# Kernel optimization log

Measured on AMD Instinct MI355X. Metric: run time of the kernel, lower is better.

The kernel has to match this reference:

```python
import jax, jax.numpy as jnp
import numpy as np

N0, N1, N2 = 360448, 22528, 2048
E0, E1 = 337920, 20480
D = 256


def setup_inputs() -> dict:
    key = jax.random.key(0)
    ks = jax.random.split(key, 12)
    s = 1.0 / np.sqrt(D)
    return {
        "x": jax.random.normal(ks[0], (N0, D), dtype=jnp.float32),
        "src0": jax.random.randint(ks[1], (E0,), 0, N0, dtype=jnp.int32),
        "dst0": jax.random.randint(ks[2], (E0,), 0, N1, dtype=jnp.int32),
        "src1": jax.random.randint(ks[3], (E1,), 0, N1, dtype=jnp.int32),
        "dst1": jax.random.randint(ks[4], (E1,), 0, N2, dtype=jnp.int32),
        "Wl0": jax.random.normal(ks[5], (D, D), dtype=jnp.float32) * s,
        "bl0": jnp.zeros((D,), dtype=jnp.float32),
        "Wr0": jax.random.normal(ks[6], (D, D), dtype=jnp.float32) * s,
        "Wl1": jax.random.normal(ks[7], (D, D), dtype=jnp.float32) * s,
        "bl1": jnp.zeros((D,), dtype=jnp.float32),
        "Wr1": jax.random.normal(ks[8], (D, D), dtype=jnp.float32) * s,
    }


def _sage_conv(x_src, x_tgt, src, dst, n_tgt, Wl, bl, Wr):
    # mean aggregation of source neighbor features per target node
    summed = jax.ops.segment_sum(x_src[src], dst, num_segments=n_tgt)
    cnt = jax.ops.segment_sum(jnp.ones((src.shape[0],), x_src.dtype), dst,
                              num_segments=n_tgt)
    agg = summed / jnp.maximum(cnt, 1.0)[:, None]
    # PyG SAGEConv: lin_l(agg) + lin_r(x_target); lin_r has no bias
    return agg @ Wl.T + bl + x_tgt @ Wr.T


def reference(x, src0, dst0, src1, dst1, Wl0, bl0, Wr0, Wl1, bl1, Wr1):
    # layer 0: [N0, D] -> [N1, D]
    h = _sage_conv(x, x[:N1], src0, dst0, N1, Wl0, bl0, Wr0)
    h = jax.nn.relu(h)  # dropout is identity in eval mode
    # layer 1: [N1, D] -> [N2, D]
    out = _sage_conv(h, h[:N2], src1, dst1, N2, Wl1, bl1, Wr1)
    return out
```

## Files before the change

### kernel.cpp

```cpp
#include <hip/hip_runtime.h>
#include <hip/hip_bf16.h>

#define N1C 22528
#define N2C 2048

typedef __attribute__((ext_vector_type(8))) short bf16x8;
typedef __attribute__((ext_vector_type(4))) float f32x4;

__device__ __forceinline__ short f2bf(float f) {
    union { float f; unsigned u; } x; x.f = f;
    unsigned r = x.u + 0x7fff + ((x.u >> 16) & 1);
    return (short)(r >> 16);
}
__device__ __forceinline__ float bf2f(unsigned short u) {
    union { unsigned u; float f; } x; x.u = ((unsigned)u) << 16;
    return x.f;
}

__global__ void prep_kernel(const float* __restrict__ Wl0, const float* __restrict__ Wr0,
                            const float* __restrict__ Wl1, const float* __restrict__ Wr1,
                            short* __restrict__ Wcat0, short* __restrict__ Wcat1,
                            int* __restrict__ hist0, int* __restrict__ hist1) {
    const int stride = gridDim.x * blockDim.x;
    const int tid0 = blockIdx.x * blockDim.x + threadIdx.x;
    for (int i = tid0; i < 2 * 256 * 512; i += stride) {
        int layer = i >> 17;
        int r = i & ((1 << 17) - 1);
        int j = r >> 9, k = r & 511;
        const float* Wl = layer ? Wl1 : Wl0;
        const float* Wr = layer ? Wr1 : Wr0;
        float v = (k < 256) ? Wl[j * 256 + k] : Wr[j * 256 + (k - 256)];
        (layer ? Wcat1 : Wcat0)[r] = f2bf(v);
    }
    for (int i = tid0; i < N1C + N2C; i += stride) {
        if (i < N1C) hist0[i] = 0; else hist1[i - N1C] = 0;
    }
}

__global__ void hist_both_kernel(const int* __restrict__ dst0, int E0,
                                 const int* __restrict__ dst1, int E1,
                                 int* __restrict__ hist0, int* __restrict__ hist1) {
    const int stride = gridDim.x * blockDim.x;
    for (int i = blockIdx.x * blockDim.x + threadIdx.x; i < E0 + E1; i += stride) {
        if (i < E0) atomicAdd(&hist0[dst0[i]], 1);
        else        atomicAdd(&hist1[dst1[i - E0]], 1);
    }
}

__global__ __launch_bounds__(1024)
void scan_both_kernel(const int* __restrict__ hist0, int* __restrict__ rowptr0,
                      int* __restrict__ cursor0,
                      const int* __restrict__ hist1, int* __restrict__ rowptr1,
                      int* __restrict__ cursor1) {
    __shared__ int sums[1024];
    const int N = (blockIdx.x == 0) ? N1C : N2C;
    const int* hist   = (blockIdx.x == 0) ? hist0 : hist1;
    int* rowptr       = (blockIdx.x == 0) ? rowptr0 : rowptr1;
    int* cursor       = (blockIdx.x == 0) ? cursor0 : cursor1;
    const int tid = threadIdx.x;
    const int per = (N + 1023) >> 10;
    const int start = tid * per;
    const int end = min(start + per, N);
    int s = 0;
    for (int i = start; i < end; ++i) s += hist[i];
    sums[tid] = s;
    __syncthreads();
    for (int d = 1; d < 1024; d <<= 1) {
        int t = (tid >= d) ? sums[tid - d] : 0;
        __syncthreads();
        sums[tid] += t;
        __syncthreads();
    }
    int off = sums[tid] - s;
    for (int i = start; i < end; ++i) {
        rowptr[i] = off;
        cursor[i] = off;
        off += hist[i];
    }
    if (tid == 1023) rowptr[N] = off;
}

__global__ void fill_both_kernel(const int* __restrict__ src0, const int* __restrict__ dst0, int E0,
                                 const int* __restrict__ src1, const int* __restrict__ dst1, int E1,
                                 int* __restrict__ cursor0, int* __restrict__ eidx0,
                                 int* __restrict__ cursor1, int* __restrict__ eidx1) {
    const int stride = gridDim.x * blockDim.x;
    for (int i = blockIdx.x * blockDim.x + threadIdx.x; i < E0 + E1; i += stride) {
        if (i < E0) {
            int p = atomicAdd(&cursor0[dst0[i]], 1);
            eidx0[p] = src0[i];
        } else {
            int p = atomicAdd(&cursor1[dst1[i - E0]], 1);
            eidx1[p] = src1[i - E0];
        }
    }
}

__global__ __launch_bounds__(256)
void gather0_kernel(const float* __restrict__ x, const int* __restrict__ rowptr,
                    const int* __restrict__ eidx, short* __restrict__ Acat0) {
    const int wv = (blockIdx.x * 256 + threadIdx.x) >> 6;
    const int lane = threadIdx.x & 63;
    if (wv >= N1C) return;

    const float4 xr = *(const float4*)(x + (size_t)wv * 256 + lane * 4);

    const int beg = rowptr[wv];
    const int end = rowptr[wv + 1];
    float4 acc = {0.f, 0.f, 0.f, 0.f};
    float4 acc2 = {0.f, 0.f, 0.f, 0.f};
    int j = beg;
    for (; j + 3 < end; j += 4) {
        const int e0 = eidx[j], e1 = eidx[j + 1], e2 = eidx[j + 2], e3 = eidx[j + 3];
        const float4 v0 = *(const float4*)(x + (size_t)e0 * 256 + lane * 4);
        const float4 v1 = *(const float4*)(x + (size_t)e1 * 256 + lane * 4);
        const float4 v2 = *(const float4*)(x + (size_t)e2 * 256 + lane * 4);
        const float4 v3 = *(const float4*)(x + (size_t)e3 * 256 + lane * 4);
        acc.x += v0.x + v1.x;  acc.y += v0.y + v1.y;
        acc.z += v0.z + v1.z;  acc.w += v0.w + v1.w;
        acc2.x += v2.x + v3.x; acc2.y += v2.y + v3.y;
        acc2.z += v2.z + v3.z; acc2.w += v2.w + v3.w;
    }
    for (; j < end; ++j) {
        const float4 v0 = *(const float4*)(x + (size_t)eidx[j] * 256 + lane * 4);
        acc.x += v0.x; acc.y += v0.y; acc.z += v0.z; acc.w += v0.w;
    }
    acc.x += acc2.x; acc.y += acc2.y; acc.z += acc2.z; acc.w += acc2.w;

    const float sc = 1.0f / fmaxf((float)(end - beg), 1.0f);
    short4 o;
    o.x = f2bf(acc.x * sc); o.y = f2bf(acc.y * sc);
    o.z = f2bf(acc.z * sc); o.w = f2bf(acc.w * sc);
    *(short4*)(Acat0 + (size_t)wv * 512 + lane * 4) = o;

    short4 xo;
    xo.x = f2bf(xr.x); xo.y = f2bf(xr.y); xo.z = f2bf(xr.z); xo.w = f2bf(xr.w);
    *(short4*)(Acat0 + (size_t)wv * 512 + 256 + lane * 4) = xo;
}

__global__ __launch_bounds__(256)
void gather1_kernel(const ushort* __restrict__ X, const int* __restrict__ rowptr,
                    const int* __restrict__ eidx, short* __restrict__ Acat, int N) {
    const int wv = (blockIdx.x * 256 + threadIdx.x) >> 6;
    const int lane = threadIdx.x & 63;
    if (wv >= N) return;
    const int beg = rowptr[wv];
    const int end = rowptr[wv + 1];
    float a0 = 0.f, a1 = 0.f, a2 = 0.f, a3 = 0.f;
    int j = beg;
    for (; j + 1 < end; j += 2) {
        int s0 = eidx[j], s1 = eidx[j + 1];
        ushort4 v0 = *(const ushort4*)(X + (size_t)s0 * 256 + lane * 4);
        ushort4 v1 = *(const ushort4*)(X + (size_t)s1 * 256 + lane * 4);
        a0 += bf2f(v0.x) + bf2f(v1.x); a1 += bf2f(v0.y) + bf2f(v1.y);
        a2 += bf2f(v0.z) + bf2f(v1.z); a3 += bf2f(v0.w) + bf2f(v1.w);
    }
    if (j < end) {
        ushort4 v0 = *(const ushort4*)(X + (size_t)eidx[j] * 256 + lane * 4);
        a0 += bf2f(v0.x); a1 += bf2f(v0.y); a2 += bf2f(v0.z); a3 += bf2f(v0.w);
    }
    const float sc = 1.0f / fmaxf((float)(end - beg), 1.0f);
    short4 o;
    o.x = f2bf(a0 * sc); o.y = f2bf(a1 * sc);
    o.z = f2bf(a2 * sc); o.w = f2bf(a3 * sc);
    *(short4*)(Acat + (size_t)wv * 512 + lane * 4) = o;
}

template <int CT, bool RELU, bool OUT_BF16>
__global__ __launch_bounds__(256)
void mfma_gemm_kernel(const short* __restrict__ A, const short* __restrict__ W,
                      const float* __restrict__ bias, void* __restrict__ out,
                      short* __restrict__ out2, int M) {
    const int tid = threadIdx.x;
    const int wave = tid >> 6;
    const int lane = tid & 63;
    const int r0 = blockIdx.x * 64 + wave * 16;
    const int j0 = blockIdx.y * (CT * 16);
    const int lrow = lane & 15;
    const int lk = (lane >> 4) * 8;

    const short* arow = A + (size_t)(r0 + lrow) * 512 + lk;
    const short* wbase = W + (size_t)(j0 + lrow) * 512 + lk;

    f32x4 acc[CT] = {};
    for (int ks = 0; ks < 16; ++ks) {
        bf16x8 a = *(const bf16x8*)(arow + ks * 32);
#pragma unroll
        for (int c = 0; c < CT; ++c) {
            bf16x8 b = *(const bf16x8*)(wbase + (size_t)c * 16 * 512 + ks * 32);
            acc[c] = __builtin_amdgcn_mfma_f32_16x16x32_bf16(a, b, acc[c], 0, 0, 0);
        }
    }

    const int orow = (lane >> 4) * 4;
#pragma unroll
    for (int c = 0; c < CT; ++c) {
        const int col = j0 + c * 16 + lrow;
        const float bv = bias[col];
#pragma unroll
        for (int i = 0; i < 4; ++i) {
            const int row = r0 + orow + i;
            float v = acc[c][i] + bv;
            if (RELU) v = fmaxf(v, 0.0f);
            if (OUT_BF16) {
                short hv = f2bf(v);
                ((short*)out)[(size_t)row * 256 + col] = hv;
                if (out2 != nullptr && row < N2C)
                    out2[(size_t)row * 512 + 256 + col] = hv;
            } else {
                ((float*)out)[(size_t)row * 256 + col] = v;
            }
        }
    }
}

extern "C" void kernel_launch(void* const* d_in, const int* in_sizes, int n_in,
                              void* d_out, int out_size, void* d_ws, size_t ws_size,
                              hipStream_t stream) {
    const float* x    = (const float*)d_in[0];
    const int*   src0 = (const int*)d_in[1];
    const int*   dst0 = (const int*)d_in[2];
    const int*   src1 = (const int*)d_in[3];
    const int*   dst1 = (const int*)d_in[4];
    const float* Wl0  = (const float*)d_in[5];
    const float* bl0  = (const float*)d_in[6];
    const float* Wr0  = (const float*)d_in[7];
    const float* Wl1  = (const float*)d_in[8];
    const float* bl1  = (const float*)d_in[9];
    const float* Wr1  = (const float*)d_in[10];

    const int E0 = in_sizes[1];
    const int E1 = in_sizes[3];

    char* p = (char*)d_ws;
    short* Acat0 = (short*)p;            p += (size_t)N1C * 512 * 2;
    short* h     = (short*)p;            p += (size_t)N1C * 256 * 2;
    short* Acat1 = (short*)p;            p += (size_t)N2C * 512 * 2;
    short* Wcat0 = (short*)p;            p += 256 * 512 * 2;
    short* Wcat1 = (short*)p;            p += 256 * 512 * 2;
    int* hist0   = (int*)p;              p += (size_t)N1C * 4;
    int* cursor0 = (int*)p;              p += (size_t)N1C * 4;
    int* rowptr0 = (int*)p;              p += (size_t)(N1C + 4) * 4;
    int* hist1   = (int*)p;              p += (size_t)N2C * 4;
    int* cursor1 = (int*)p;              p += (size_t)N2C * 4;
    int* rowptr1 = (int*)p;              p += (size_t)(N2C + 4) * 4;
    int* eidx0   = (int*)p;              p += (size_t)E0 * 4;
    int* eidx1   = (int*)p;              p += (size_t)E1 * 4;

    prep_kernel<<<512, 256, 0, stream>>>(Wl0, Wr0, Wl1, Wr1, Wcat0, Wcat1, hist0, hist1);
    hist_both_kernel<<<512, 256, 0, stream>>>(dst0, E0, dst1, E1, hist0, hist1);
    scan_both_kernel<<<2, 1024, 0, stream>>>(hist0, rowptr0, cursor0, hist1, rowptr1, cursor1);
    fill_both_kernel<<<512, 256, 0, stream>>>(src0, dst0, E0, src1, dst1, E1,
                                              cursor0, eidx0, cursor1, eidx1);
    gather0_kernel<<<(N1C * 64 + 255) / 256, 256, 0, stream>>>(x, rowptr0, eidx0, Acat0);
    mfma_gemm_kernel<16, true, true><<<dim3(N1C / 64, 1), 256, 0, stream>>>(
        Acat0, Wcat0, bl0, h, Acat1, N1C);
    gather1_kernel<<<(N2C * 64 + 255) / 256, 256, 0, stream>>>(
        (const ushort*)h, rowptr1, eidx1, Acat1, N2C);
    mfma_gemm_kernel<4, false, false><<<dim3(N2C / 64, 4), 256, 0, stream>>>(
        Acat1, Wcat1, bl1, (float*)d_out, nullptr, N2C);
}
```

Before: 231.7 us.

## Pre-convert x to bf16, fuse layer-1 gather with GEMM, retile GEMM0

Adds a pass in the prep kernel that converts all of x to bf16 so the layer-0 gather reads half-width rows. Fuses the layer-1 mean aggregation into the layer-1 GEMM through shared memory, which removes a kernel and the Acat1 round trip. Splits the layer-0 GEMM into four column tiles per row block. The full conversion of x reads and writes far more data than the gather touches, so it adds substantial memory traffic.

```diff
diff --git a/kernel.cpp b/kernel.cpp
--- a/kernel.cpp
+++ b/kernel.cpp
@@ -1,11 +1,13 @@
 #include <hip/hip_runtime.h>
 #include <hip/hip_bf16.h>
 
+#define N0C 360448
 #define N1C 22528
 #define N2C 2048
 
 typedef __attribute__((ext_vector_type(8))) short bf16x8;
 typedef __attribute__((ext_vector_type(4))) float f32x4;
+typedef __attribute__((ext_vector_type(4))) float nt_f32x4;
 
 __device__ __forceinline__ short f2bf(float f) {
     union { float f; unsigned u; } x; x.f = f;
@@ -17,13 +19,15 @@
     return x.f;
 }
 
-__global__ void prep_kernel(const float* __restrict__ Wl0, const float* __restrict__ Wr0,
-                            const float* __restrict__ Wl1, const float* __restrict__ Wr1,
-                            short* __restrict__ Wcat0, short* __restrict__ Wcat1,
-                            int* __restrict__ hist0, int* __restrict__ hist1) {
+__global__ __launch_bounds__(256)
+void prep_all_kernel(const float* __restrict__ Wl0, const float* __restrict__ Wr0,
+                     const float* __restrict__ Wl1, const float* __restrict__ Wr1,
+                     short* __restrict__ Wcat0, short* __restrict__ Wcat1,
+                     int* __restrict__ hist0, int* __restrict__ hist1,
+                     const float* __restrict__ x, ushort* __restrict__ xb) {
     const int stride = gridDim.x * blockDim.x;
-    const int tid0 = blockIdx.x * blockDim.x + threadIdx.x;
-    for (int i = tid0; i < 2 * 256 * 512; i += stride) {
+    const int t0 = blockIdx.x * blockDim.x + threadIdx.x;
+    for (int i = t0; i < 2 * 256 * 512; i += stride) {
         int layer = i >> 17;
         int r = i & ((1 << 17) - 1);
         int j = r >> 9, k = r & 511;
@@ -32,8 +36,16 @@
         float v = (k < 256) ? Wl[j * 256 + k] : Wr[j * 256 + (k - 256)];
         (layer ? Wcat1 : Wcat0)[r] = f2bf(v);
     }
-    for (int i = tid0; i < N1C + N2C; i += stride) {
+    for (int i = t0; i < N1C + N2C; i += stride) {
         if (i < N1C) hist0[i] = 0; else hist1[i - N1C] = 0;
+    }
+    const long long total = (long long)N0C * 64;
+    for (long long u = t0; u < total; u += stride) {
+        nt_f32x4 v = __builtin_nontemporal_load((const nt_f32x4*)x + u);
+        ushort4 o;
+        o.x = (ushort)f2bf(v.x); o.y = (ushort)f2bf(v.y);
+        o.z = (ushort)f2bf(v.z); o.w = (ushort)f2bf(v.w);
+        *((ushort4*)xb + u) = o;
     }
 }
 
@@ -97,96 +109,64 @@
 }
 
 __global__ __launch_bounds__(256)
-void gather0_kernel(const float* __restrict__ x, const int* __restrict__ rowptr,
+void gather0_kernel(const ushort* __restrict__ xb, const int* __restrict__ rowptr,
                     const int* __restrict__ eidx, short* __restrict__ Acat0) {
     const int wv = (blockIdx.x * 256 + threadIdx.x) >> 6;
     const int lane = threadIdx.x & 63;
     if (wv >= N1C) return;
 
-    const float4 xr = *(const float4*)(x + (size_t)wv * 256 + lane * 4);
+    const ushort4 xr = *(const ushort4*)(xb + (size_t)wv * 256 + lane * 4);
 
     const int beg = rowptr[wv];
     const int end = rowptr[wv + 1];
-    float4 acc = {0.f, 0.f, 0.f, 0.f};
-    float4 acc2 = {0.f, 0.f, 0.f, 0.f};
+    float a0 = 0.f, a1 = 0.f, a2 = 0.f, a3 = 0.f;
+    float b0 = 0.f, b1 = 0.f, b2 = 0.f, b3 = 0.f;
     int j = beg;
     for (; j + 3 < end; j += 4) {
         const int e0 = eidx[j], e1 = eidx[j + 1], e2 = eidx[j + 2], e3 = eidx[j + 3];
-        const float4 v0 = *(const float4*)(x + (size_t)e0 * 256 + lane * 4);
-        const float4 v1 = *(const float4*)(x + (size_t)e1 * 256 + lane * 4);
-        const float4 v2 = *(const float4*)(x + (size_t)e2 * 256 + lane * 4);
-        const float4 v3 = *(const float4*)(x + (size_t)e3 * 256 + lane * 4);
-        acc.x += v0.x + v1.x;  acc.y += v0.y + v1.y;
-        acc.z += v0.z + v1.z;  acc.w += v0.w + v1.w;
-        acc2.x += v2.x + v3.x; acc2.y += v2.y + v3.y;
-        acc2.z += v2.z + v3.z; acc2.w += v2.w + v3.w;
-    }
-    for (; j < end; ++j) {
-        const float4 v0 = *(const float4*)(x + (size_t)eidx[j] * 256 + lane * 4);
-        acc.x += v0.x; acc.y += v0.y; acc.z += v0.z; acc.w += v0.w;
-    }
-    acc.x += acc2.x; acc.y += acc2.y; acc.z += acc2.z; acc.w += acc2.w;
-
-    const float sc = 1.0f / fmaxf((float)(end - beg), 1.0f);
-    short4 o;
-    o.x = f2bf(acc.x * sc); o.y = f2bf(acc.y * sc);
-    o.z = f2bf(acc.z * sc); o.w = f2bf(acc.w * sc);
-    *(short4*)(Acat0 + (size_t)wv * 512 + lane * 4) = o;
-
-    short4 xo;
-    xo.x = f2bf(xr.x); xo.y = f2bf(xr.y); xo.z = f2bf(xr.z); xo.w = f2bf(xr.w);
-    *(short4*)(Acat0 + (size_t)wv * 512 + 256 + lane * 4) = xo;
-}
-
-__global__ __launch_bounds__(256)
-void gather1_kernel(const ushort* __restrict__ X, const int* __restrict__ rowptr,
-                    const int* __restrict__ eidx, short* __restrict__ Acat, int N) {
-    const int wv = (blockIdx.x * 256 + threadIdx.x) >> 6;
-    const int lane = threadIdx.x & 63;
-    if (wv >= N) return;
-    const int beg = rowptr[wv];
-    const int end = rowptr[wv + 1];
-    float a0 = 0.f, a1 = 0.f, a2 = 0.f, a3 = 0.f;
-    int j = beg;
-    for (; j + 1 < end; j += 2) {
-        int s0 = eidx[j], s1 = eidx[j + 1];
-        ushort4 v0 = *(const ushort4*)(X + (size_t)s0 * 256 + lane * 4);
-        ushort4 v1 = *(const ushort4*)(X + (size_t)s1 * 256 + lane * 4);
+        const ushort4 v0 = *(const ushort4*)(xb + (size_t)e0 * 256 + lane * 4);
+        const ushort4 v1 = *(const ushort4*)(xb + (size_t)e1 * 256 + lane * 4);
+        const ushort4 v2 = *(const ushort4*)(xb + (size_t)e2 * 256 + lane * 4);
+        const ushort4 v3 = *(const ushort4*)(xb + (size_t)e3 * 256 + lane * 4);
         a0 += bf2f(v0.x) + bf2f(v1.x); a1 += bf2f(v0.y) + bf2f(v1.y);
         a2 += bf2f(v0.z) + bf2f(v1.z); a3 += bf2f(v0.w) + bf2f(v1.w);
-    }
-    if (j < end) {
-        ushort4 v0 = *(const ushort4*)(X + (size_t)eidx[j] * 256 + lane * 4);
+        b0 += bf2f(v2.x) + bf2f(v3.x); b1 += bf2f(v2.y) + bf2f(v3.y);
+        b2 += bf2f(v2.z) + bf2f(v3.z); b3 += bf2f(v2.w) + bf2f(v3.w);
+    }
+    for (; j < end; ++j) {
+        const ushort4 v0 = *(const ushort4*)(xb + (size_t)eidx[j] * 256 + lane * 4);
         a0 += bf2f(v0.x); a1 += bf2f(v0.y); a2 += bf2f(v0.z); a3 += bf2f(v0.w);
     }
+    a0 += b0; a1 += b1; a2 += b2; a3 += b3;
+
     const float sc = 1.0f / fmaxf((float)(end - beg), 1.0f);
     short4 o;
     o.x = f2bf(a0 * sc); o.y = f2bf(a1 * sc);
     o.z = f2bf(a2 * sc); o.w = f2bf(a3 * sc);
-    *(short4*)(Acat + (size_t)wv * 512 + lane * 4) = o;
-}
-
-template <int CT, bool RELU, bool OUT_BF16>
+    *(short4*)(Acat0 + (size_t)wv * 512 + lane * 4) = o;
+    *(ushort4*)(Acat0 + (size_t)wv * 512 + 256 + lane * 4) = xr;
+}
+
 __global__ __launch_bounds__(256)
-void mfma_gemm_kernel(const short* __restrict__ A, const short* __restrict__ W,
-                      const float* __restrict__ bias, void* __restrict__ out,
-                      short* __restrict__ out2, int M) {
+void mfma_gemm0_kernel(const short* __restrict__ A, const short* __restrict__ W,
+                       const float* __restrict__ bias, short* __restrict__ out) {
     const int tid = threadIdx.x;
     const int wave = tid >> 6;
     const int lane = tid & 63;
     const int r0 = blockIdx.x * 64 + wave * 16;
-    const int j0 = blockIdx.y * (CT * 16);
+    const int j0 = blockIdx.y * 64;
     const int lrow = lane & 15;
     const int lk = (lane >> 4) * 8;
 
     const short* arow = A + (size_t)(r0 + lrow) * 512 + lk;
     const short* wbase = W + (size_t)(j0 + lrow) * 512 + lk;
 
-    f32x4 acc[CT] = {};
+    f32x4 acc[4] = {};
+#pragma unroll
     for (int ks = 0; ks < 16; ++ks) {
         bf16x8 a = *(const bf16x8*)(arow + ks * 32);
 #pragma unroll
-        for (int c = 0; c < CT; ++c) {
+        for (int c = 0; c < 4; ++c) {
             bf16x8 b = *(const bf16x8*)(wbase + (size_t)c * 16 * 512 + ks * 32);
             acc[c] = __builtin_amdgcn_mfma_f32_16x16x32_bf16(a, b, acc[c], 0, 0, 0);
         }
@@ -194,22 +174,82 @@
 
     const int orow = (lane >> 4) * 4;
 #pragma unroll
-    for (int c = 0; c < CT; ++c) {
+    for (int c = 0; c < 4; ++c) {
         const int col = j0 + c * 16 + lrow;
         const float bv = bias[col];
 #pragma unroll
         for (int i = 0; i < 4; ++i) {
             const int row = r0 + orow + i;
-            float v = acc[c][i] + bv;
-            if (RELU) v = fmaxf(v, 0.0f);
-            if (OUT_BF16) {
-                short hv = f2bf(v);
-                ((short*)out)[(size_t)row * 256 + col] = hv;
-                if (out2 != nullptr && row < N2C)
-                    out2[(size_t)row * 512 + 256 + col] = hv;
-            } else {
-                ((float*)out)[(size_t)row * 256 + col] = v;
-            }
+            float v = fmaxf(acc[c][i] + bv, 0.0f);
+            out[(size_t)row * 256 + col] = f2bf(v);
+        }
+    }
+}
+
+__global__ __launch_bounds__(256)
+void sage1_fused_kernel(const ushort* __restrict__ h, const int* __restrict__ rowptr,
+                        const int* __restrict__ eidx, const short* __restrict__ W,
+                        const float* __restrict__ bias, float* __restrict__ out) {
+    __shared__ short As[64][520];
+
+    const int tid = threadIdx.x;
+    const int wave = tid >> 6;
+    const int lane = tid & 63;
+    const int rbase = blockIdx.x * 64;
+
+    for (int i = 0; i < 16; ++i) {
+        const int lr = wave * 16 + i;
+        const int node = rbase + lr;
+        const int beg = rowptr[node];
+        const int end = rowptr[node + 1];
+        float a0 = 0.f, a1 = 0.f, a2 = 0.f, a3 = 0.f;
+        int j = beg;
+        for (; j + 1 < end; j += 2) {
+            const int s0 = eidx[j], s1 = eidx[j + 1];
+            const ushort4 v0 = *(const ushort4*)(h + (size_t)s0 * 256 + lane * 4);
+            const ushort4 v1 = *(const ushort4*)(h + (size_t)s1 * 256 + lane * 4);
+            a0 += bf2f(v0.x) + bf2f(v1.x); a1 += bf2f(v0.y) + bf2f(v1.y);
+            a2 += bf2f(v0.z) + bf2f(v1.z); a3 += bf2f(v0.w) + bf2f(v1.w);
+        }
+        if (j < end) {
+            const ushort4 v0 = *(const ushort4*)(h + (size_t)eidx[j] * 256 + lane * 4);
+            a0 += bf2f(v0.x); a1 += bf2f(v0.y); a2 += bf2f(v0.z); a3 += bf2f(v0.w);
+        }
+        const float sc = 1.0f / fmaxf((float)(end - beg), 1.0f);
+        short4 o;
+        o.x = f2bf(a0 * sc); o.y = f2bf(a1 * sc);
+        o.z = f2bf(a2 * sc); o.w = f2bf(a3 * sc);
+        *(short4*)&As[lr][lane * 4] = o;
+        const ushort4 hr = *(const ushort4*)(h + (size_t)node * 256 + lane * 4);
+        *(ushort4*)&As[lr][256 + lane * 4] = hr;
+    }
+    __syncthreads();
+
+    const int lrow = lane & 15;
+    const int lk = (lane >> 4) * 8;
+    const short* arow = &As[wave * 16 + lrow][lk];
+    const short* wbase = W + (size_t)lrow * 512 + lk;
+
+    f32x4 acc[16] = {};
+#pragma unroll
+    for (int ks = 0; ks < 16; ++ks) {
+        bf16x8 a = *(const bf16x8*)(arow + ks * 32);
+#pragma unroll
+        for (int c = 0; c < 16; ++c) {
+            bf16x8 b = *(const bf16x8*)(wbase + (size_t)c * 16 * 512 + ks * 32);
+            acc[c] = __builtin_amdgcn_mfma_f32_16x16x32_bf16(a, b, acc[c], 0, 0, 0);
+        }
+    }
+
+    const int orow = (lane >> 4) * 4;
+#pragma unroll
+    for (int c = 0; c < 16; ++c) {
+        const int col = c * 16 + lrow;
+        const float bv = bias[col];
+#pragma unroll
+        for (int i = 0; i < 4; ++i) {
+            const int row = rbase + wave * 16 + orow + i;
+            out[(size_t)row * 256 + col] = acc[c][i] + bv;
         }
     }
 }
@@ -233,9 +273,9 @@
     const int E1 = in_sizes[3];
 
     char* p = (char*)d_ws;
+    ushort* xb   = (ushort*)p;           p += (size_t)N0C * 256 * 2;
     short* Acat0 = (short*)p;            p += (size_t)N1C * 512 * 2;
     short* h     = (short*)p;            p += (size_t)N1C * 256 * 2;
-    short* Acat1 = (short*)p;            p += (size_t)N2C * 512 * 2;
     short* Wcat0 = (short*)p;            p += 256 * 512 * 2;
     short* Wcat1 = (short*)p;            p += 256 * 512 * 2;
     int* hist0   = (int*)p;              p += (size_t)N1C * 4;
@@ -247,16 +287,14 @@
     int* eidx0   = (int*)p;              p += (size_t)E0 * 4;
     int* eidx1   = (int*)p;              p += (size_t)E1 * 4;
 
-    prep_kernel<<<512, 256, 0, stream>>>(Wl0, Wr0, Wl1, Wr1, Wcat0, Wcat1, hist0, hist1);
+    prep_all_kernel<<<2048, 256, 0, stream>>>(Wl0, Wr0, Wl1, Wr1, Wcat0, Wcat1,
+                                              hist0, hist1, x, xb);
     hist_both_kernel<<<512, 256, 0, stream>>>(dst0, E0, dst1, E1, hist0, hist1);
     scan_both_kernel<<<2, 1024, 0, stream>>>(hist0, rowptr0, cursor0, hist1, rowptr1, cursor1);
     fill_both_kernel<<<512, 256, 0, stream>>>(src0, dst0, E0, src1, dst1, E1,
                                               cursor0, eidx0, cursor1, eidx1);
-    gather0_kernel<<<(N1C * 64 + 255) / 256, 256, 0, stream>>>(x, rowptr0, eidx0, Acat0);
-    mfma_gemm_kernel<16, true, true><<<dim3(N1C / 64, 1), 256, 0, stream>>>(
-        Acat0, Wcat0, bl0, h, Acat1, N1C);
-    gather1_kernel<<<(N2C * 64 + 255) / 256, 256, 0, stream>>>(
-        (const ushort*)h, rowptr1, eidx1, Acat1, N2C);
-    mfma_gemm_kernel<4, false, false><<<dim3(N2C / 64, 4), 256, 0, stream>>>(
-        Acat1, Wcat1, bl1, (float*)d_out, nullptr, N2C);
-}
+    gather0_kernel<<<(N1C * 64 + 255) / 256, 256, 0, stream>>>(xb, rowptr0, eidx0, Acat0);
+    mfma_gemm0_kernel<<<dim3(N1C / 64, 4), 256, 0, stream>>>(Acat0, Wcat0, bl0, h);
+    sage1_fused_kernel<<<N2C / 64, 256, 0, stream>>>((const ushort*)h, rowptr1, eidx1,
+                                                     Wcat1, bl1, (float*)d_out);
+}
```

Result: slower. 363.9 us (+57.0%).
